# Optimization experiments

Hardware: AMD Instinct MI355X
Metric: run time of the kernel (lower is better)

## Reference

```python
import jax, jax.numpy as jnp
import numpy as np

M = 8192
A_N, A_K = 64, 64  # out_factors[0], in_factors[0]
B_N, B_K = 64, 64  # out_factors[1], in_factors[1]
K = A_K * B_K
N = A_N * B_N


def setup_inputs() -> dict:
    key = jax.random.key(0)
    kx, ka, kb, kbias = jax.random.split(key, 4)
    x = jax.random.normal(kx, (M, K), dtype=jnp.float32)
    A = jax.random.normal(ka, (A_N, A_K), dtype=jnp.float32) * (1.0 / np.sqrt(A_K))
    B = jax.random.normal(kb, (B_N, B_K), dtype=jnp.float32) * (1.0 / np.sqrt(B_K))
    bias = jax.random.normal(kbias, (N,), dtype=jnp.float32) * 0.01
    return {"x": x, "A": A, "B": B, "bias": bias}


def reference(x, A, B, bias):
    # Y = X @ (A kron B)^T + bias, computed without materializing A kron B.
    # Column index n of the kron weight decomposes as n = p*B_N + q with
    # (A kron B)[n, k] = A[p, k//B_K] * B[q, k%B_K].
    m, k = x.shape
    a_n, a_k = A.shape
    b_n, b_k = B.shape
    xr = x.reshape(m, a_k, b_k)                    # [M, A_K, B_K]
    y = jnp.einsum('mab,qb->maq', xr, B)           # contract B factor
    y = jnp.einsum('maq,pa->mpq', y, A)            # contract A factor
    return y.reshape(m, a_n * b_n) + bias[None, :]
```

## Files before the change

### kernel.cpp

```cpp
#include <hip/hip_runtime.h>

typedef __attribute__((ext_vector_type(8))) short short8v;
typedef __attribute__((ext_vector_type(4))) short short4v;
typedef __attribute__((ext_vector_type(4))) float float4v;

__device__ __forceinline__ short f2bf(float f) {
  __bf16 h = (__bf16)f;
  return __builtin_bit_cast(short, h);
}

__device__ __forceinline__ short8v load_frag8(const float* __restrict__ p) {
  float4 a = *reinterpret_cast<const float4*>(p);
  float4 b = *reinterpret_cast<const float4*>(p + 4);
  short8v r;
  r[0] = f2bf(a.x); r[1] = f2bf(a.y); r[2] = f2bf(a.z); r[3] = f2bf(a.w);
  r[4] = f2bf(b.x); r[5] = f2bf(b.y); r[6] = f2bf(b.z); r[7] = f2bf(b.w);
  return r;
}

__device__ __forceinline__ void stage_weight(const float* __restrict__ src,
                                             short* __restrict__ dst, int tid) {
  const int r = tid >> 2;
  const int c0 = (tid & 3) << 4;
  const float* p = src + r * 64 + c0;
  float4 f0 = reinterpret_cast<const float4*>(p)[0];
  float4 f1 = reinterpret_cast<const float4*>(p)[1];
  float4 f2 = reinterpret_cast<const float4*>(p)[2];
  float4 f3 = reinterpret_cast<const float4*>(p)[3];
  short8v g0, g1;
  g0[0] = f2bf(f0.x); g0[1] = f2bf(f0.y); g0[2] = f2bf(f0.z); g0[3] = f2bf(f0.w);
  g0[4] = f2bf(f1.x); g0[5] = f2bf(f1.y); g0[6] = f2bf(f1.z); g0[7] = f2bf(f1.w);
  g1[0] = f2bf(f2.x); g1[1] = f2bf(f2.y); g1[2] = f2bf(f2.z); g1[3] = f2bf(f2.w);
  g1[4] = f2bf(f3.x); g1[5] = f2bf(f3.y); g1[6] = f2bf(f3.z); g1[7] = f2bf(f3.w);
  const int sw = (r & 7) << 3;
  *reinterpret_cast<short8v*>(&dst[r * 64 + ((c0)     ^ sw)]) = g0;
  *reinterpret_cast<short8v*>(&dst[r * 64 + ((c0 + 8) ^ sw)]) = g1;
}

__global__ __launch_bounds__(256, 3)
void kron64_kernel(const float* __restrict__ x, const float* __restrict__ A,
                   const float* __restrict__ B, const float* __restrict__ bias,
                   float* __restrict__ out) {
  __shared__ short bw[4096];
  __shared__ short aw[4096];
  __shared__ short y1[4][4096];

  const int tid = threadIdx.x;
  const int w = tid >> 6;
  const int lane = tid & 63;
  const int g = lane >> 4;
  const int c = lane & 15;
  const int swz = (c & 7) << 3;

  stage_weight(B, bw, tid);
  stage_weight(A, aw, tid);
  __syncthreads();

  const int m = blockIdx.x * 4 + w;
  const float* xm = x + (size_t)m * 4096;
  short* yw = y1[w];
  const float4v vzero = {0.f, 0.f, 0.f, 0.f};

  {
    short8v bfr[4][2];
#pragma unroll
    for (int qt = 0; qt < 4; ++qt)
#pragma unroll
      for (int kk = 0; kk < 2; ++kk)
        bfr[qt][kk] = *reinterpret_cast<const short8v*>(
            &bw[(16 * qt + c) * 64 + ((32 * kk + 8 * g) ^ swz)]);

#pragma unroll
    for (int at = 0; at < 4; ++at) {
      float4v acc[4];
#pragma unroll
      for (int qt = 0; qt < 4; ++qt) acc[qt] = vzero;
#pragma unroll
      for (int kk = 0; kk < 2; ++kk) {
        short8v xfrag = load_frag8(xm + (16 * at + c) * 64 + 32 * kk + 8 * g);
#pragma unroll
        for (int qt = 0; qt < 4; ++qt)
          acc[qt] = __builtin_amdgcn_mfma_f32_16x16x32_bf16(
              xfrag, bfr[qt][kk], acc[qt], 0, 0, 0);
      }
#pragma unroll
      for (int qt = 0; qt < 4; ++qt) {
        short4v v;
        v[0] = f2bf(acc[qt][0]); v[1] = f2bf(acc[qt][1]);
        v[2] = f2bf(acc[qt][2]); v[3] = f2bf(acc[qt][3]);
        int idx = ((16 * qt + c) * 64 + 16 * at + 4 * g) ^ swz;
        *reinterpret_cast<short4v*>(&yw[idx]) = v;
      }
    }
  }

  __asm__ volatile("s_waitcnt lgkmcnt(0)" ::: "memory");

  {
    short8v yfr[4][2];
#pragma unroll
    for (int qt = 0; qt < 4; ++qt)
#pragma unroll
      for (int kk = 0; kk < 2; ++kk) {
        int idx = (((16 * qt + c) * 64) + 32 * kk + 8 * g) ^ swz;
        yfr[qt][kk] = *reinterpret_cast<const short8v*>(&yw[idx]);
      }

    float* om = out + (size_t)m * 4096;
#pragma unroll
    for (int pt = 0; pt < 4; ++pt) {
      short8v afr[2];
#pragma unroll
      for (int kk = 0; kk < 2; ++kk)
        afr[kk] = *reinterpret_cast<const short8v*>(
            &aw[(16 * pt + c) * 64 + ((32 * kk + 8 * g) ^ swz)]);
#pragma unroll
      for (int qt = 0; qt < 4; ++qt) {
        const int n = (16 * pt + c) * 64 + 16 * qt + 4 * g;
        float4 bv = *reinterpret_cast<const float4*>(bias + n);
        float4v acc; acc[0] = bv.x; acc[1] = bv.y; acc[2] = bv.z; acc[3] = bv.w;
#pragma unroll
        for (int kk = 0; kk < 2; ++kk)
          acc = __builtin_amdgcn_mfma_f32_16x16x32_bf16(
              yfr[qt][kk], afr[kk], acc, 0, 0, 0);
        *reinterpret_cast<float4v*>(om + n) = acc;
      }
    }
  }
}

extern "C" void kernel_launch(void* const* d_in, const int* in_sizes, int n_in,
                              void* d_out, int out_size, void* d_ws, size_t ws_size,
                              hipStream_t stream) {
  (void)in_sizes; (void)n_in; (void)out_size; (void)d_ws; (void)ws_size;
  const float* x    = (const float*)d_in[0];
  const float* A    = (const float*)d_in[1];
  const float* B    = (const float*)d_in[2];
  const float* bias = (const float*)d_in[3];
  float* out = (float*)d_out;

  dim3 grid(2048), block(256);
  hipLaunchKernelGGL(kron64_kernel, grid, block, 0, stream, x, A, B, bias, out);
}
```

Measured before the change: 57.33 us.

## Split each row across two waves and prefetch x before weight staging barrier

Each block now handles two rows instead of four, with two waves cooperating on one row. Each wave computes half of the first-stage tiles and half of the second-stage output columns, with a block barrier between the stages. The x loads for each wave are issued before the weight-staging barrier so global latency overlaps the LDS staging. B fragments are reloaded from LDS inside the loop to save registers. Halving LDS use and raising the occupancy hint aims at more resident blocks, at the cost of double the grid size, redundant weight staging per block and an extra barrier.

```diff
diff --git a/kernel.cpp b/kernel.cpp
--- a/kernel.cpp
+++ b/kernel.cpp
@@ -9,9 +9,7 @@
   return __builtin_bit_cast(short, h);
 }
 
-__device__ __forceinline__ short8v load_frag8(const float* __restrict__ p) {
-  float4 a = *reinterpret_cast<const float4*>(p);
-  float4 b = *reinterpret_cast<const float4*>(p + 4);
+__device__ __forceinline__ short8v cvt8(float4 a, float4 b) {
   short8v r;
   r[0] = f2bf(a.x); r[1] = f2bf(a.y); r[2] = f2bf(a.z); r[3] = f2bf(a.w);
   r[4] = f2bf(b.x); r[5] = f2bf(b.y); r[6] = f2bf(b.z); r[7] = f2bf(b.w);
@@ -27,23 +25,19 @@
   float4 f1 = reinterpret_cast<const float4*>(p)[1];
   float4 f2 = reinterpret_cast<const float4*>(p)[2];
   float4 f3 = reinterpret_cast<const float4*>(p)[3];
-  short8v g0, g1;
-  g0[0] = f2bf(f0.x); g0[1] = f2bf(f0.y); g0[2] = f2bf(f0.z); g0[3] = f2bf(f0.w);
-  g0[4] = f2bf(f1.x); g0[5] = f2bf(f1.y); g0[6] = f2bf(f1.z); g0[7] = f2bf(f1.w);
-  g1[0] = f2bf(f2.x); g1[1] = f2bf(f2.y); g1[2] = f2bf(f2.z); g1[3] = f2bf(f2.w);
-  g1[4] = f2bf(f3.x); g1[5] = f2bf(f3.y); g1[6] = f2bf(f3.z); g1[7] = f2bf(f3.w);
+  short8v g0 = cvt8(f0, f1), g1 = cvt8(f2, f3);
   const int sw = (r & 7) << 3;
   *reinterpret_cast<short8v*>(&dst[r * 64 + ((c0)     ^ sw)]) = g0;
   *reinterpret_cast<short8v*>(&dst[r * 64 + ((c0 + 8) ^ sw)]) = g1;
 }
 
-__global__ __launch_bounds__(256, 3)
+__global__ __launch_bounds__(256, 4)
 void kron64_kernel(const float* __restrict__ x, const float* __restrict__ A,
                    const float* __restrict__ B, const float* __restrict__ bias,
                    float* __restrict__ out) {
   __shared__ short bw[4096];
   __shared__ short aw[4096];
-  __shared__ short y1[4][4096];
+  __shared__ short y1[2][4096];
 
   const int tid = threadIdx.x;
   const int w = tid >> 6;
@@ -54,56 +48,67 @@
 
   stage_weight(B, bw, tid);
   stage_weight(A, aw, tid);
+
+  const int rs = w >> 1;
+  const int half = w & 1;
+  const int m = blockIdx.x * 2 + rs;
+  const float* xm = x + (size_t)m * 4096;
+  short* yw = y1[rs];
+  const float4v vzero = {0.f, 0.f, 0.f, 0.f};
+
+  const int A0 = 2 * half;
+  float4 xb[8];
+  {
+    const float* base = xm + (16 * A0 + c) * 64 + 8 * g;
+#pragma unroll
+    for (int atl = 0; atl < 2; ++atl)
+#pragma unroll
+      for (int kk = 0; kk < 2; ++kk) {
+        const float* p = base + atl * 1024 + kk * 32;
+        xb[(atl * 2 + kk) * 2 + 0] = reinterpret_cast<const float4*>(p)[0];
+        xb[(atl * 2 + kk) * 2 + 1] = reinterpret_cast<const float4*>(p)[1];
+      }
+  }
+
   __syncthreads();
 
-  const int m = blockIdx.x * 4 + w;
-  const float* xm = x + (size_t)m * 4096;
-  short* yw = y1[w];
-  const float4v vzero = {0.f, 0.f, 0.f, 0.f};
-
-  {
-    short8v bfr[4][2];
 #pragma unroll
-    for (int qt = 0; qt < 4; ++qt)
+  for (int atl = 0; atl < 2; ++atl) {
+    const int at = A0 + atl;
+    float4v acc[4];
 #pragma unroll
-      for (int kk = 0; kk < 2; ++kk)
-        bfr[qt][kk] = *reinterpret_cast<const short8v*>(
-            &bw[(16 * qt + c) * 64 + ((32 * kk + 8 * g) ^ swz)]);
-
+    for (int qt = 0; qt < 4; ++qt) acc[qt] = vzero;
 #pragma unroll
-    for (int at = 0; at < 4; ++at) {
-      float4v acc[4];
-#pragma unroll
-      for (int qt = 0; qt < 4; ++qt) acc[qt] = vzero;
-#pragma unroll
-      for (int kk = 0; kk < 2; ++kk) {
-        short8v xfrag = load_frag8(xm + (16 * at + c) * 64 + 32 * kk + 8 * g);
-#pragma unroll
-        for (int qt = 0; qt < 4; ++qt)
-          acc[qt] = __builtin_amdgcn_mfma_f32_16x16x32_bf16(
-              xfrag, bfr[qt][kk], acc[qt], 0, 0, 0);
-      }
+    for (int kk = 0; kk < 2; ++kk) {
+      short8v xf = cvt8(xb[(atl * 2 + kk) * 2], xb[(atl * 2 + kk) * 2 + 1]);
 #pragma unroll
       for (int qt = 0; qt < 4; ++qt) {
-        short4v v;
-        v[0] = f2bf(acc[qt][0]); v[1] = f2bf(acc[qt][1]);
-        v[2] = f2bf(acc[qt][2]); v[3] = f2bf(acc[qt][3]);
-        int idx = ((16 * qt + c) * 64 + 16 * at + 4 * g) ^ swz;
-        *reinterpret_cast<short4v*>(&yw[idx]) = v;
+        short8v bfrk = *reinterpret_cast<const short8v*>(
+            &bw[(16 * qt + c) * 64 + ((32 * kk + 8 * g) ^ swz)]);
+        acc[qt] = __builtin_amdgcn_mfma_f32_16x16x32_bf16(
+            xf, bfrk, acc[qt], 0, 0, 0);
       }
+    }
+#pragma unroll
+    for (int qt = 0; qt < 4; ++qt) {
+      short4v v;
+      v[0] = f2bf(acc[qt][0]); v[1] = f2bf(acc[qt][1]);
+      v[2] = f2bf(acc[qt][2]); v[3] = f2bf(acc[qt][3]);
+      int idx = ((16 * qt + c) * 64 + 16 * at + 4 * g) ^ swz;
+      *reinterpret_cast<short4v*>(&yw[idx]) = v;
     }
   }
 
-  __asm__ volatile("s_waitcnt lgkmcnt(0)" ::: "memory");
+  __syncthreads();
 
   {
-    short8v yfr[4][2];
+    short8v yfr[2][2];
 #pragma unroll
-    for (int qt = 0; qt < 4; ++qt)
+    for (int qtl = 0; qtl < 2; ++qtl)
 #pragma unroll
       for (int kk = 0; kk < 2; ++kk) {
-        int idx = (((16 * qt + c) * 64) + 32 * kk + 8 * g) ^ swz;
-        yfr[qt][kk] = *reinterpret_cast<const short8v*>(&yw[idx]);
+        int idx = ((16 * (2 * half + qtl) + c) * 64) + ((32 * kk + 8 * g) ^ swz);
+        yfr[qtl][kk] = *reinterpret_cast<const short8v*>(&yw[idx]);
       }
 
     float* om = out + (size_t)m * 4096;
@@ -115,14 +120,14 @@
         afr[kk] = *reinterpret_cast<const short8v*>(
             &aw[(16 * pt + c) * 64 + ((32 * kk + 8 * g) ^ swz)]);
 #pragma unroll
-      for (int qt = 0; qt < 4; ++qt) {
-        const int n = (16 * pt + c) * 64 + 16 * qt + 4 * g;
+      for (int qtl = 0; qtl < 2; ++qtl) {
+        const int n = (16 * pt + c) * 64 + 16 * (2 * half + qtl) + 4 * g;
         float4 bv = *reinterpret_cast<const float4*>(bias + n);
         float4v acc; acc[0] = bv.x; acc[1] = bv.y; acc[2] = bv.z; acc[3] = bv.w;
 #pragma unroll
         for (int kk = 0; kk < 2; ++kk)
           acc = __builtin_amdgcn_mfma_f32_16x16x32_bf16(
-              yfr[qt][kk], afr[kk], acc, 0, 0, 0);
+              yfr[qtl][kk], afr[kk], acc, 0, 0, 0);
         *reinterpret_cast<float4v*>(om + n) = acc;
       }
     }
@@ -139,6 +144,6 @@
   const float* bias = (const float*)d_in[3];
   float* out = (float*)d_out;
 
-  dim3 grid(2048), block(256);
+  dim3 grid(4096), block(256);
   hipLaunchKernelGGL(kron64_kernel, grid, block, 0, stream, x, A, B, bias, out);
 }
```

Measured after the change: 55.45 us. 3.3% less time.
